# Performance work log

Hardware: AMD Instinct MI355X
Metric: run time of the kernel (lower is better)

Reference implementation:

```python
import jax, jax.numpy as jnp
import numpy as np

V, D, H, DH, FF, L = 512, 256, 8, 32, 2048, 2
B, S = 4, 128
EPS = 1e-5


def setup_inputs() -> dict:
    key = jax.random.key(0)
    ks = jax.random.split(key, 8)
    rn = lambda k, shape: jax.random.normal(k, shape, jnp.float32) * 0.02
    return {
        "x_t": jax.random.randint(ks[0], (B, S), 0, V),
        "emb": rn(ks[1], (V, D)),
        "temperature": jnp.array(1.0, jnp.float32),
        "Wq": rn(ks[2], (L, D, D)), "Wk": rn(ks[3], (L, D, D)),
        "Wv": rn(ks[4], (L, D, D)), "Wo": rn(ks[5], (L, D, D)),
        "bq": jnp.zeros((L, D)), "bk": jnp.zeros((L, D)),
        "bv": jnp.zeros((L, D)), "bo": jnp.zeros((L, D)),
        "W1": rn(ks[6], (L, D, FF)), "b1": jnp.zeros((L, FF)),
        "W2": rn(ks[7], (L, FF, D)), "b2": jnp.zeros((L, D)),
        "ln1_s": jnp.ones((L, D)), "ln1_b": jnp.zeros((L, D)),
        "ln2_s": jnp.ones((L, D)), "ln2_b": jnp.zeros((L, D)),
    }


def _layer_norm(x, scale, bias):
    m = jnp.mean(x, axis=-1, keepdims=True)
    v = jnp.var(x, axis=-1, keepdims=True)
    return (x - m) / jnp.sqrt(v + EPS) * scale + bias


def reference(x_t, emb, temperature, Wq, Wk, Wv, Wo, bq, bk, bv, bo,
              W1, b1, W2, b2, ln1_s, ln1_b, ln2_s, ln2_b):
    b, s = x_t.shape
    x = emb[x_t]  # [B,S,D]
    scale = 1.0 / np.sqrt(DH).astype(np.float32)
    for l in range(L):  # 2 structurally distinct layers (post-norm, ReLU FFN)
        q = (x @ Wq[l] + bq[l]).reshape(b, s, H, DH)
        k = (x @ Wk[l] + bk[l]).reshape(b, s, H, DH)
        v = (x @ Wv[l] + bv[l]).reshape(b, s, H, DH)
        scores = jnp.einsum('bqhd,bkhd->bhqk', q, k) * scale
        attn = jax.nn.softmax(scores, axis=-1)
        o = jnp.einsum('bhqk,bkhd->bqhd', attn, v).reshape(b, s, D)
        x = _layer_norm(x + (o @ Wo[l] + bo[l]), ln1_s[l], ln1_b[l])
        ff = jax.nn.relu(x @ W1[l] + b1[l]) @ W2[l] + b2[l]
        x = _layer_norm(x + ff, ln2_s[l], ln2_b[l])
    sim = (x @ emb.T) / temperature            # [B,S,V]
    tp = jax.nn.softmax(sim, axis=-1)          # [B,S,V]
    # torch loop `trans_matrix[:,:,i,:] = transition_probs` == broadcast over row dim
    return jnp.broadcast_to(tp[:, :, None, :], (b, s, V, V))
```

## Files before the change

### kernel.cpp

```cpp
#include <hip/hip_runtime.h>
#include <math.h>

#define V_  512
#define D_  256
#define H_  8
#define DH_ 32
#define FF_ 2048
#define L_  2
#define B_  4
#define S_  128
#define T_  (B_*S_)

typedef float f32x4 __attribute__((ext_vector_type(4)));
typedef short s16x8 __attribute__((ext_vector_type(8)));
typedef unsigned short u16x4 __attribute__((ext_vector_type(4)));
typedef unsigned short ushort_t;

__device__ __forceinline__ ushort_t f2b(float f) {
    unsigned int u = __builtin_bit_cast(unsigned int, f);
    u += 0x7FFFu + ((u >> 16) & 1u);
    return (ushort_t)(u >> 16);
}
__device__ __forceinline__ float b2f(ushort_t h) {
    unsigned int u = ((unsigned int)h) << 16;
    return __builtin_bit_cast(float, u);
}

__device__ __forceinline__ float waveReduceSum(float v) {
#pragma unroll
    for (int off = 32; off > 0; off >>= 1) v += __shfl_xor(v, off);
    return v;
}
__device__ __forceinline__ float waveReduceMax(float v) {
#pragma unroll
    for (int off = 32; off > 0; off >>= 1) v = fmaxf(v, __shfl_xor(v, off));
    return v;
}

template<int RELU, int OUTB, int BIAS>
__device__ __forceinline__ void mgemm_body(
    const ushort_t* __restrict__ A, const ushort_t* __restrict__ BT,
    const float* __restrict__ bias, float* __restrict__ Cf,
    ushort_t* __restrict__ Cb, int M, int N, int K, int kBegin, int kSteps)
{
    __shared__ ushort_t Al[2][64][72];
    __shared__ ushort_t Bl[2][64][72];
    const int tid  = threadIdx.x;
    const int m0   = blockIdx.y * 64, n0 = blockIdx.x * 64;
    const int lane = tid & 63, w = tid >> 6;
    const int srow = tid >> 2, sseg = (tid & 3) * 16;
    const int l15  = lane & 15,  kg = (lane >> 4) * 8;

    f32x4 acc0 = {0.f,0.f,0.f,0.f}, acc1 = acc0, acc2 = acc0, acc3 = acc0;

    const ushort_t* Aptr = &A [(size_t)(m0 + srow) * K + kBegin + sseg];
    const ushort_t* Bptr = &BT[(size_t)(n0 + srow) * K + kBegin + sseg];

    s16x8 av0 = *(const s16x8*)Aptr,       av1 = *(const s16x8*)(Aptr + 8);
    s16x8 bv0 = *(const s16x8*)Bptr,       bv1 = *(const s16x8*)(Bptr + 8);
    *(s16x8*)&Al[0][srow][sseg]     = av0;
    *(s16x8*)&Al[0][srow][sseg + 8] = av1;
    *(s16x8*)&Bl[0][srow][sseg]     = bv0;
    *(s16x8*)&Bl[0][srow][sseg + 8] = bv1;

    for (int kt = 0; kt < kSteps; ++kt) {
        const int cur = kt & 1;
        const bool more = (kt + 1 < kSteps);
        if (more) {
            const size_t o = (size_t)(kt + 1) * 64;
            av0 = *(const s16x8*)(Aptr + o);     av1 = *(const s16x8*)(Aptr + o + 8);
            bv0 = *(const s16x8*)(Bptr + o);     bv1 = *(const s16x8*)(Bptr + o + 8);
        }
        asm volatile("s_waitcnt lgkmcnt(0)\n\ts_barrier" ::: "memory");

        s16x8 b0 = *(const s16x8*)&Bl[cur][w * 16 + l15][kg];
        s16x8 b1 = *(const s16x8*)&Bl[cur][w * 16 + l15][kg + 32];
        s16x8 a00 = *(const s16x8*)&Al[cur][     l15][kg];
        s16x8 a01 = *(const s16x8*)&Al[cur][     l15][kg + 32];
        s16x8 a10 = *(const s16x8*)&Al[cur][16 + l15][kg];
        s16x8 a11 = *(const s16x8*)&Al[cur][16 + l15][kg + 32];
        s16x8 a20 = *(const s16x8*)&Al[cur][32 + l15][kg];
        s16x8 a21 = *(const s16x8*)&Al[cur][32 + l15][kg + 32];
        s16x8 a30 = *(const s16x8*)&Al[cur][48 + l15][kg];
        s16x8 a31 = *(const s16x8*)&Al[cur][48 + l15][kg + 32];
        acc0 = __builtin_amdgcn_mfma_f32_16x16x32_bf16(a00, b0, acc0, 0, 0, 0);
        acc1 = __builtin_amdgcn_mfma_f32_16x16x32_bf16(a10, b0, acc1, 0, 0, 0);
        acc2 = __builtin_amdgcn_mfma_f32_16x16x32_bf16(a20, b0, acc2, 0, 0, 0);
        acc3 = __builtin_amdgcn_mfma_f32_16x16x32_bf16(a30, b0, acc3, 0, 0, 0);
        acc0 = __builtin_amdgcn_mfma_f32_16x16x32_bf16(a01, b1, acc0, 0, 0, 0);
        acc1 = __builtin_amdgcn_mfma_f32_16x16x32_bf16(a11, b1, acc1, 0, 0, 0);
        acc2 = __builtin_amdgcn_mfma_f32_16x16x32_bf16(a21, b1, acc2, 0, 0, 0);
        acc3 = __builtin_amdgcn_mfma_f32_16x16x32_bf16(a31, b1, acc3, 0, 0, 0);

        if (more) {
            *(s16x8*)&Al[cur ^ 1][srow][sseg]     = av0;
            *(s16x8*)&Al[cur ^ 1][srow][sseg + 8] = av1;
            *(s16x8*)&Bl[cur ^ 1][srow][sseg]     = bv0;
            *(s16x8*)&Bl[cur ^ 1][srow][sseg + 8] = bv1;
        }
    }

    const int col = n0 + w * 16 + l15;
    const float bb = BIAS ? bias[col] : 0.f;
    f32x4 accs[4] = {acc0, acc1, acc2, acc3};
#pragma unroll
    for (int r = 0; r < 4; ++r) {
#pragma unroll
        for (int e = 0; e < 4; ++e) {
            const int row = m0 + r * 16 + (lane >> 4) * 4 + e;
            float v = accs[r][e] + bb;
            if (RELU) v = fmaxf(v, 0.f);
            if (OUTB) Cb[(size_t)row * N + col] = f2b(v);
            else      Cf[(size_t)row * N + col] = v;
        }
    }
}

template<int RELU, int OUTB, int BIAS>
__global__ __launch_bounds__(256) void mgemm_k(const ushort_t* A, const ushort_t* BT,
    const float* bias, float* Cf0, float* Cf1, ushort_t* Cb,
    int M, int N, int K, int kChunk)
{
    const int z = blockIdx.z;
    float* Cfz = nullptr;
    if (Cf0) Cfz = (z < 2) ? Cf0 + (size_t)z * M * N
                           : Cf1 + (size_t)(z - 2) * M * N;
    mgemm_body<RELU, OUTB, BIAS>(A, BT, bias, Cfz, Cb, M, N, K,
                                 z * kChunk, kChunk / 64);
}

__global__ __launch_bounds__(256) void qkv_k(const ushort_t* Xb, const ushort_t* WT,
    const float* bq, const float* bk, const float* bv,
    ushort_t* Qb, ushort_t* Kb, ushort_t* Vb)
{
    const int z = blockIdx.z;
    const ushort_t* bt = WT + (size_t)z * (D_ * D_);
    const float* bias; ushort_t* out;
    if (z == 0)      { bias = bq; out = Qb; }
    else if (z == 1) { bias = bk; out = Kb; }
    else             { bias = bv; out = Vb; }
    mgemm_body<0, 1, 1>(Xb, bt, bias, nullptr, out, T_, D_, D_, 0, D_ / 64);
}

__global__ __launch_bounds__(256) void prep_k(const int* __restrict__ xt,
    const float* __restrict__ emb, float* __restrict__ X,
    ushort_t* __restrict__ Xb, ushort_t* __restrict__ embB,
    const float* __restrict__ Wq, const float* __restrict__ Wk,
    const float* __restrict__ Wv, const float* __restrict__ Wo,
    const float* __restrict__ W1, const float* __restrict__ W2,
    ushort_t* __restrict__ WT, ushort_t* __restrict__ W1T, ushort_t* __restrict__ W2T)
{
    __shared__ float Tl[32][33];
    const int tid = threadIdx.x;
    if (blockIdx.x < 512) {
        const int idx = blockIdx.x * 256 + tid;
        const int t = idx >> 8, d = idx & 255;
        const float v = emb[(size_t)xt[t] * D_ + d];
        X[idx]  = v;
        Xb[idx] = f2b(v);
        embB[idx] = f2b(emb[idx]);
        return;
    }
    const int id = blockIdx.x - 512;
    const int l  = id >= 1280 ? 1 : 0;
    const int t  = id - l * 1280;
    const float* src; ushort_t* dst; int R, C, rt, ct;
    if (t < 256) {
        const int kind = t >> 6, tl = t & 63;
        const float* s0 = (kind == 0) ? Wq : (kind == 1) ? Wk : (kind == 2) ? Wv : Wo;
        src = s0 + (size_t)l * (D_ * D_);
        dst = WT + (size_t)l * (4 * D_ * D_) + (size_t)kind * (D_ * D_);
        R = D_; C = D_; rt = tl >> 3; ct = tl & 7;
    } else if (t < 768) {
        const int tl = t - 256;
        src = W1 + (size_t)l * (D_ * FF_); dst = W1T + (size_t)l * (D_ * FF_);
        R = D_; C = FF_; rt = tl >> 6; ct = tl & 63;
    } else {
        const int tl = t - 768;
        src = W2 + (size_t)l * (FF_ * D_); dst = W2T + (size_t)l * (FF_ * D_);
        R = FF_; C = D_; rt = tl >> 3; ct = tl & 7;
    }
    const int r = tid >> 3, c4 = (tid & 7) * 4;
    f32x4 v = *(const f32x4*)&src[(size_t)(rt * 32 + r) * C + ct * 32 + c4];
    Tl[r][c4] = v[0]; Tl[r][c4 + 1] = v[1]; Tl[r][c4 + 2] = v[2]; Tl[r][c4 + 3] = v[3];
    __syncthreads();
    u16x4 ov;
    ov[0] = f2b(Tl[c4 + 0][r]); ov[1] = f2b(Tl[c4 + 1][r]);
    ov[2] = f2b(Tl[c4 + 2][r]); ov[3] = f2b(Tl[c4 + 3][r]);
    *(u16x4*)&dst[(size_t)(ct * 32 + r) * R + rt * 32 + c4] = ov;
}

__global__ __launch_bounds__(256) void add_ln_k(
    const float* __restrict__ p0, const float* __restrict__ p1, int nparts,
    const float* __restrict__ bias, float* __restrict__ X,
    ushort_t* __restrict__ Xb, const float* __restrict__ s,
    const float* __restrict__ b)
{
    __shared__ float red[4];
    const int row = blockIdx.x, tid = threadIdx.x;
    const size_t off = (size_t)row * D_ + tid;
    const size_t TD = (size_t)T_ * D_;
    float a = X[off] + bias[tid] + p0[off];
    if (nparts >= 2) a += p0[TD + off];
    if (nparts == 4) a += p1[off] + p1[TD + off];

    float ws_ = waveReduceSum(a);
    if ((tid & 63) == 0) red[tid >> 6] = ws_;
    __syncthreads();
    const float mean = (red[0] + red[1] + red[2] + red[3]) * (1.f / D_);
    __syncthreads();
    const float d = a - mean;
    float vs = waveReduceSum(d * d);
    if ((tid & 63) == 0) red[tid >> 6] = vs;
    __syncthreads();
    const float var = (red[0] + red[1] + red[2] + red[3]) * (1.f / D_);
    const float y = d * rsqrtf(var + 1e-5f) * s[tid] + b[tid];
    X[off]  = y;
    Xb[off] = f2b(y);
}

__global__ __launch_bounds__(256) void attn_k(const ushort_t* __restrict__ Qb,
    const ushort_t* __restrict__ Kb, const ushort_t* __restrict__ Vb,
    ushort_t* __restrict__ Ob)
{
    __shared__ float Qs[32][36], Ks[128][36], Vs[128][36], Ps[32][132];
    const int bh = blockIdx.x, b = bh >> 3, h = bh & 7;
    const int i0 = blockIdx.y * 32;
    const int tid = threadIdx.x;

#pragma unroll
    for (int it = 0; it < 2; ++it) {
        const int g = it * 256 + tid;
        const int r = g >> 2, c8 = (g & 3) * 8;
        s16x8 kv = *(const s16x8*)&Kb[(size_t)(b * S_ + r) * D_ + h * DH_ + c8];
        s16x8 vv = *(const s16x8*)&Vb[(size_t)(b * S_ + r) * D_ + h * DH_ + c8];
        f32x4 klo = {b2f((ushort_t)kv[0]), b2f((ushort_t)kv[1]), b2f((ushort_t)kv[2]), b2f((ushort_t)kv[3])};
        f32x4 khi = {b2f((ushort_t)kv[4]), b2f((ushort_t)kv[5]), b2f((ushort_t)kv[6]), b2f((ushort_t)kv[7])};
        f32x4 vlo = {b2f((ushort_t)vv[0]), b2f((ushort_t)vv[1]), b2f((ushort_t)vv[2]), b2f((ushort_t)vv[3])};
        f32x4 vhi = {b2f((ushort_t)vv[4]), b2f((ushort_t)vv[5]), b2f((ushort_t)vv[6]), b2f((ushort_t)vv[7])};
        *(f32x4*)&Ks[r][c8]     = klo;  *(f32x4*)&Ks[r][c8 + 4] = khi;
        *(f32x4*)&Vs[r][c8]     = vlo;  *(f32x4*)&Vs[r][c8 + 4] = vhi;
    }
    if (tid < 128) {
        const int r = tid >> 2, c8 = (tid & 3) * 8;
        s16x8 qv = *(const s16x8*)&Qb[(size_t)(b * S_ + i0 + r) * D_ + h * DH_ + c8];
        f32x4 qlo = {b2f((ushort_t)qv[0]), b2f((ushort_t)qv[1]), b2f((ushort_t)qv[2]), b2f((ushort_t)qv[3])};
        f32x4 qhi = {b2f((ushort_t)qv[4]), b2f((ushort_t)qv[5]), b2f((ushort_t)qv[6]), b2f((ushort_t)qv[7])};
        *(f32x4*)&Qs[r][c8] = qlo;  *(f32x4*)&Qs[r][c8 + 4] = qhi;
    }
    __syncthreads();

    const int i = tid >> 3, jg = tid & 7;
    const float sc = 0.17677669529663687f;
    float sv[16];
    float mx = -1e30f;
#pragma unroll
    for (int jj = 0; jj < 16; ++jj) {
        const int j = jg + jj * 8;
        f32x4 a4 = {0.f,0.f,0.f,0.f};
#pragma unroll
        for (int kk = 0; kk < 8; ++kk) {
            f32x4 q = *(const f32x4*)&Qs[i][kk * 4];
            f32x4 k = *(const f32x4*)&Ks[j][kk * 4];
            a4 += q * k;
        }
        const float sdot = (a4[0] + a4[1] + a4[2] + a4[3]) * sc;
        sv[jj] = sdot;
        mx = fmaxf(mx, sdot);
    }
    mx = fmaxf(mx, __shfl_xor(mx, 1));
    mx = fmaxf(mx, __shfl_xor(mx, 2));
    mx = fmaxf(mx, __shfl_xor(mx, 4));
    float sum = 0.f;
#pragma unroll
    for (int jj = 0; jj < 16; ++jj) {
        const float e = __expf(sv[jj] - mx);
        Ps[i][jg + jj * 8] = e;
        sum += e;
    }
    sum += __shfl_xor(sum, 1);
    sum += __shfl_xor(sum, 2);
    sum += __shfl_xor(sum, 4);
    const float inv = 1.f / sum;
    __syncthreads();

    const int dg = tid & 7;
    f32x4 o = {0.f,0.f,0.f,0.f};
#pragma unroll 4
    for (int j = 0; j < 128; ++j) {
        const float p = Ps[i][j];
        f32x4 vv = *(const f32x4*)&Vs[j][dg * 4];
        o += vv * p;
    }
    u16x4 ov;
    ov[0] = f2b(o[0] * inv); ov[1] = f2b(o[1] * inv);
    ov[2] = f2b(o[2] * inv); ov[3] = f2b(o[3] * inv);
    *(u16x4*)&Ob[(size_t)(b * S_ + i0 + i) * D_ + h * DH_ + dg * 4] = ov;
}

__global__ __launch_bounds__(256) void bcast_k(const float* __restrict__ Lg,
    const float* __restrict__ temp, float* __restrict__ out)
{
    __shared__ float row[V_];
    __shared__ float red[4];
    const int blk = blockIdx.x, t = blk >> 2, quarter = blk & 3;
    const int tid = threadIdx.x;
    const float rT = 1.f / temp[0];
    const float l0 = Lg[(size_t)t * V_ + tid] * rT;
    const float l1 = Lg[(size_t)t * V_ + 256 + tid] * rT;
    float m = waveReduceMax(fmaxf(l0, l1));
    if ((tid & 63) == 0) red[tid >> 6] = m;
    __syncthreads();
    m = fmaxf(fmaxf(red[0], red[1]), fmaxf(red[2], red[3]));
    __syncthreads();
    const float e0 = __expf(l0 - m), e1 = __expf(l1 - m);
    float sblk = waveReduceSum(e0 + e1);
    if ((tid & 63) == 0) red[tid >> 6] = sblk;
    __syncthreads();
    const float inv = 1.f / (red[0] + red[1] + red[2] + red[3]);
    row[tid] = e0 * inv;
    row[tid + 256] = e1 * inv;
    __syncthreads();

    const int c = tid & 127, ihalf = tid >> 7;
    f32x4 v = *(const f32x4*)&row[c * 4];
    f32x4* dst = (f32x4*)out + (size_t)t * V_ * (V_ / 4);
#pragma unroll 4
    for (int r = 0; r < 64; ++r) {
        const int i = quarter * 128 + ihalf + r * 2;
        __builtin_nontemporal_store(v, &dst[(size_t)i * (V_ / 4) + c]);
    }
}

extern "C" void kernel_launch(void* const* d_in, const int* in_sizes, int n_in,
                              void* d_out, int out_size, void* d_ws, size_t ws_size,
                              hipStream_t stream)
{
    const int*   x_t  = (const int*)  d_in[0];
    const float* emb  = (const float*)d_in[1];
    const float* temp = (const float*)d_in[2];
    const float* Wq   = (const float*)d_in[3];
    const float* Wk   = (const float*)d_in[4];
    const float* Wv   = (const float*)d_in[5];
    const float* Wo   = (const float*)d_in[6];
    const float* bq   = (const float*)d_in[7];
    const float* bk   = (const float*)d_in[8];
    const float* bv   = (const float*)d_in[9];
    const float* bo   = (const float*)d_in[10];
    const float* W1   = (const float*)d_in[11];
    const float* b1   = (const float*)d_in[12];
    const float* W2   = (const float*)d_in[13];
    const float* b2   = (const float*)d_in[14];
    const float* ln1s = (const float*)d_in[15];
    const float* ln1b = (const float*)d_in[16];
    const float* ln2s = (const float*)d_in[17];
    const float* ln2b = (const float*)d_in[18];

    float* out = (float*)d_out;
    char*  wsb = (char*)d_ws;

    float*    X     = (float*)   (wsb + 0);
    float*    PartA = (float*)   (wsb + 524288);
    float*    Lg    = PartA;
    ushort_t* Qb    = (ushort_t*)(wsb + 1572864);
    float*    PartB = (float*)   (wsb + 1572864);
    ushort_t* Kb    = (ushort_t*)(wsb + 1835008);
    ushort_t* Vb    = (ushort_t*)(wsb + 2097152);
    ushort_t* Ob    = (ushort_t*)(wsb + 2359296);
    ushort_t* Xb    = (ushort_t*)(wsb + 2621440);
    ushort_t* Ffb   = (ushort_t*)(wsb + 2883584);
    ushort_t* embB  = (ushort_t*)(wsb + 4980736);
    ushort_t* WT    = (ushort_t*)(wsb + 5242880);
    ushort_t* W1T   = (ushort_t*)(wsb + 6291456);
    ushort_t* W2T   = (ushort_t*)(wsb + 8388608);

    prep_k<<<3072, 256, 0, stream>>>(x_t, emb, X, Xb, embB,
                                     Wq, Wk, Wv, Wo, W1, W2, WT, W1T, W2T);

    for (int l = 0; l < L_; ++l) {
        const ushort_t* WTl  = WT  + (size_t)l * (4 * D_ * D_);
        const ushort_t* W1Tl = W1T + (size_t)l * (D_ * FF_);
        const ushort_t* W2Tl = W2T + (size_t)l * (FF_ * D_);

        qkv_k<<<dim3(4, 8, 3), 256, 0, stream>>>(
            Xb, WTl, bq + l * D_, bk + l * D_, bv + l * D_, Qb, Kb, Vb);

        attn_k<<<dim3(32, 4), 256, 0, stream>>>(Qb, Kb, Vb, Ob);

        mgemm_k<0, 0, 0><<<dim3(4, 8, 2), 256, 0, stream>>>(
            Ob, WTl + 3 * D_ * D_, nullptr, PartA, nullptr, nullptr,
            T_, D_, D_, D_ / 2);
        add_ln_k<<<T_, 256, 0, stream>>>(PartA, nullptr, 2, bo + l * D_,
                                         X, Xb, ln1s + l * D_, ln1b + l * D_);

        mgemm_k<1, 1, 1><<<dim3(32, 8, 1), 256, 0, stream>>>(
            Xb, W1Tl, b1 + l * FF_, nullptr, nullptr, Ffb, T_, FF_, D_, D_);

        mgemm_k<0, 0, 0><<<dim3(4, 8, 4), 256, 0, stream>>>(
            Ffb, W2Tl, nullptr, PartA, PartB, nullptr, T_, D_, FF_, FF_ / 4);
        add_ln_k<<<T_, 256, 0, stream>>>(PartA, PartB, 4, b2 + l * D_,
                                         X, Xb, ln2s + l * D_, ln2b + l * D_);
    }

    mgemm_k<0, 0, 0><<<dim3(8, 8, 1), 256, 0, stream>>>(
        Xb, embB, nullptr, Lg, nullptr, nullptr, T_, V_, D_, D_);

    bcast_k<<<T_ * 4, 256, 0, stream>>>(Lg, temp, out);
}
```

Baseline: 172.6 us.

## Fuse QKV projection into attention and Wo GEMM into residual LayerNorm

```diff
diff --git a/kernel.cpp b/kernel.cpp
--- a/kernel.cpp
+++ b/kernel.cpp
@@ -129,17 +129,183 @@
                                  z * kChunk, kChunk / 64);
 }
 
-__global__ __launch_bounds__(256) void qkv_k(const ushort_t* Xb, const ushort_t* WT,
-    const float* bq, const float* bk, const float* bv,
-    ushort_t* Qb, ushort_t* Kb, ushort_t* Vb)
-{
-    const int z = blockIdx.z;
-    const ushort_t* bt = WT + (size_t)z * (D_ * D_);
-    const float* bias; ushort_t* out;
-    if (z == 0)      { bias = bq; out = Qb; }
-    else if (z == 1) { bias = bk; out = Kb; }
-    else             { bias = bv; out = Vb; }
-    mgemm_body<0, 1, 1>(Xb, bt, bias, nullptr, out, T_, D_, D_, 0, D_ / 64);
+__global__ __launch_bounds__(512) void qkvattn_k(
+    const ushort_t* __restrict__ Xb, const ushort_t* __restrict__ WT,
+    const float* __restrict__ bq, const float* __restrict__ bk,
+    const float* __restrict__ bv, ushort_t* __restrict__ Ob)
+{
+    __shared__ float Qs[128][36], Ks[128][36], Vs[128][36];
+    const int bh = blockIdx.x, b = bh >> 3, h = bh & 7;
+    const int tid = threadIdx.x;
+    const int w = tid >> 6, lane = tid & 63;
+    const int l15 = lane & 15, kg = (lane >> 4) * 8;
+
+    {
+        const ushort_t* WB; const float* bias; float (*dst)[36];
+        int rowbase, nrf;
+        if (w < 4)      { WB = WT;               bias = bq; dst = Qs; rowbase = w * 32;       nrf = 2; }
+        else if (w < 6) { WB = WT + D_ * D_;     bias = bk; dst = Ks; rowbase = (w - 4) * 64; nrf = 4; }
+        else            { WB = WT + 2 * D_ * D_; bias = bv; dst = Vs; rowbase = (w - 6) * 64; nrf = 4; }
+
+        f32x4 acc[4][2] = {};
+        const ushort_t* Abase = Xb + (size_t)(b * S_ + rowbase) * D_;
+        const ushort_t* Bbase = WB + (size_t)(h * DH_) * D_;
+#pragma unroll
+        for (int kk = 0; kk < 8; ++kk) {
+            const int k0 = kk * 32 + kg;
+            s16x8 bf0 = *(const s16x8*)&Bbase[(size_t)l15 * D_ + k0];
+            s16x8 bf1 = *(const s16x8*)&Bbase[(size_t)(16 + l15) * D_ + k0];
+#pragma unroll
+            for (int rf = 0; rf < 4; ++rf) {
+                if (rf < nrf) {
+                    s16x8 af = *(const s16x8*)&Abase[(size_t)(rf * 16 + l15) * D_ + k0];
+                    acc[rf][0] = __builtin_amdgcn_mfma_f32_16x16x32_bf16(af, bf0, acc[rf][0], 0, 0, 0);
+                    acc[rf][1] = __builtin_amdgcn_mfma_f32_16x16x32_bf16(af, bf1, acc[rf][1], 0, 0, 0);
+                }
+            }
+        }
+        const int r0 = (lane >> 4) * 4;
+#pragma unroll
+        for (int rf = 0; rf < 4; ++rf) {
+            if (rf < nrf) {
+#pragma unroll
+                for (int cf = 0; cf < 2; ++cf) {
+                    const int col = cf * 16 + l15;
+                    const float bb = bias[h * DH_ + col];
+#pragma unroll
+                    for (int e = 0; e < 4; ++e)
+                        dst[rowbase + rf * 16 + r0 + e][col] = acc[rf][cf][e] + bb;
+                }
+            }
+        }
+    }
+    __syncthreads();
+
+    const int i = tid >> 2, jg = tid & 3;
+    const float sc = 0.17677669529663687f;
+    float p[32];
+    float mx = -1e30f;
+#pragma unroll
+    for (int jj = 0; jj < 32; ++jj) {
+        const int j = jg + jj * 4;
+        f32x4 a4 = {0.f, 0.f, 0.f, 0.f};
+#pragma unroll
+        for (int k4 = 0; k4 < 8; ++k4) {
+            f32x4 q  = *(const f32x4*)&Qs[i][k4 * 4];
+            f32x4 kv = *(const f32x4*)&Ks[j][k4 * 4];
+            a4 += q * kv;
+        }
+        const float s = (a4[0] + a4[1] + a4[2] + a4[3]) * sc;
+        p[jj] = s;
+        mx = fmaxf(mx, s);
+    }
+    mx = fmaxf(mx, __shfl_xor(mx, 1));
+    mx = fmaxf(mx, __shfl_xor(mx, 2));
+    float sum = 0.f;
+#pragma unroll
+    for (int jj = 0; jj < 32; ++jj) {
+        p[jj] = __expf(p[jj] - mx);
+        sum += p[jj];
+    }
+    sum += __shfl_xor(sum, 1);
+    sum += __shfl_xor(sum, 2);
+    const float inv = 1.f / sum;
+
+    f32x4 o[8] = {};
+#pragma unroll
+    for (int jj = 0; jj < 32; ++jj) {
+        const int j = jg + jj * 4;
+        const float pv = p[jj];
+#pragma unroll
+        for (int d4 = 0; d4 < 8; ++d4) {
+            f32x4 vv = *(const f32x4*)&Vs[j][d4 * 4];
+            o[d4] += vv * pv;
+        }
+    }
+#pragma unroll
+    for (int d4 = 0; d4 < 8; ++d4) {
+#pragma unroll
+        for (int e = 0; e < 4; ++e) {
+            o[d4][e] += __shfl_xor(o[d4][e], 1);
+            o[d4][e] += __shfl_xor(o[d4][e], 2);
+        }
+    }
+    const int d0 = jg * 2;
+    s16x8 ov;
+#pragma unroll
+    for (int e = 0; e < 4; ++e) {
+        ov[e]     = (short)f2b(o[d0][e] * inv);
+        ov[4 + e] = (short)f2b(o[d0 + 1][e] * inv);
+    }
+    *(s16x8*)&Ob[(size_t)(b * S_ + i) * D_ + h * DH_ + jg * 8] = ov;
+}
+
+__global__ __launch_bounds__(512) void woln_k(
+    const ushort_t* __restrict__ A,
+    const ushort_t* __restrict__ BT,
+    const float* __restrict__ bias,
+    float* __restrict__ X, ushort_t* __restrict__ Xb,
+    const float* __restrict__ lns, const float* __restrict__ lnb)
+{
+    __shared__ float Ct[16][264];
+    const int tid = threadIdx.x;
+    const int m0 = blockIdx.x * 16;
+    const int w = tid >> 6, lane = tid & 63;
+    const int l15 = lane & 15, kg = (lane >> 4) * 8;
+
+    f32x4 acc0 = {0.f,0.f,0.f,0.f}, acc1 = acc0;
+    const ushort_t* Abase = A  + (size_t)(m0 + l15) * D_;
+    const ushort_t* B0    = BT + (size_t)(w * 32 + l15) * D_;
+    const ushort_t* B1    = BT + (size_t)(w * 32 + 16 + l15) * D_;
+#pragma unroll
+    for (int kk = 0; kk < 8; ++kk) {
+        const int k0 = kk * 32 + kg;
+        s16x8 af = *(const s16x8*)&Abase[k0];
+        s16x8 b0 = *(const s16x8*)&B0[k0];
+        s16x8 b1 = *(const s16x8*)&B1[k0];
+        acc0 = __builtin_amdgcn_mfma_f32_16x16x32_bf16(af, b0, acc0, 0, 0, 0);
+        acc1 = __builtin_amdgcn_mfma_f32_16x16x32_bf16(af, b1, acc1, 0, 0, 0);
+    }
+    const int r0 = (lane >> 4) * 4;
+#pragma unroll
+    for (int e = 0; e < 4; ++e) {
+        Ct[r0 + e][w * 32 + l15]      = acc0[e];
+        Ct[r0 + e][w * 32 + 16 + l15] = acc1[e];
+    }
+    __syncthreads();
+
+    const int row = tid >> 5, cg = tid & 31;
+    const int grow = m0 + row, c0 = cg * 8;
+    float a[8];
+    float sum = 0.f;
+#pragma unroll
+    for (int e = 0; e < 8; ++e) {
+        a[e] = Ct[row][c0 + e] + X[(size_t)grow * D_ + c0 + e] + bias[c0 + e];
+        sum += a[e];
+    }
+    sum += __shfl_xor(sum, 1);  sum += __shfl_xor(sum, 2);
+    sum += __shfl_xor(sum, 4);  sum += __shfl_xor(sum, 8);
+    sum += __shfl_xor(sum, 16);
+    const float mean = sum * (1.f / D_);
+    float vs = 0.f;
+#pragma unroll
+    for (int e = 0; e < 8; ++e) { const float d = a[e] - mean; vs += d * d; }
+    vs += __shfl_xor(vs, 1);  vs += __shfl_xor(vs, 2);
+    vs += __shfl_xor(vs, 4);  vs += __shfl_xor(vs, 8);
+    vs += __shfl_xor(vs, 16);
+    const float rstd = rsqrtf(vs * (1.f / D_) + 1e-5f);
+    f32x4 y0, y1; u16x4 yb0, yb1;
+#pragma unroll
+    for (int e = 0; e < 4; ++e) {
+        const float ya = (a[e] - mean) * rstd * lns[c0 + e] + lnb[c0 + e];
+        const float yc = (a[e + 4] - mean) * rstd * lns[c0 + 4 + e] + lnb[c0 + 4 + e];
+        y0[e] = ya; yb0[e] = f2b(ya);
+        y1[e] = yc; yb1[e] = f2b(yc);
+    }
+    *(f32x4*)&X [(size_t)grow * D_ + c0]     = y0;
+    *(f32x4*)&X [(size_t)grow * D_ + c0 + 4] = y1;
+    *(u16x4*)&Xb[(size_t)grow * D_ + c0]     = yb0;
+    *(u16x4*)&Xb[(size_t)grow * D_ + c0 + 4] = yb1;
 }
 
 __global__ __launch_bounds__(256) void prep_k(const int* __restrict__ xt,
@@ -217,85 +383,6 @@
     const float y = d * rsqrtf(var + 1e-5f) * s[tid] + b[tid];
     X[off]  = y;
     Xb[off] = f2b(y);
-}
-
-__global__ __launch_bounds__(256) void attn_k(const ushort_t* __restrict__ Qb,
-    const ushort_t* __restrict__ Kb, const ushort_t* __restrict__ Vb,
-    ushort_t* __restrict__ Ob)
-{
-    __shared__ float Qs[32][36], Ks[128][36], Vs[128][36], Ps[32][132];
-    const int bh = blockIdx.x, b = bh >> 3, h = bh & 7;
-    const int i0 = blockIdx.y * 32;
-    const int tid = threadIdx.x;
-
-#pragma unroll
-    for (int it = 0; it < 2; ++it) {
-        const int g = it * 256 + tid;
-        const int r = g >> 2, c8 = (g & 3) * 8;
-        s16x8 kv = *(const s16x8*)&Kb[(size_t)(b * S_ + r) * D_ + h * DH_ + c8];
-        s16x8 vv = *(const s16x8*)&Vb[(size_t)(b * S_ + r) * D_ + h * DH_ + c8];
-        f32x4 klo = {b2f((ushort_t)kv[0]), b2f((ushort_t)kv[1]), b2f((ushort_t)kv[2]), b2f((ushort_t)kv[3])};
-        f32x4 khi = {b2f((ushort_t)kv[4]), b2f((ushort_t)kv[5]), b2f((ushort_t)kv[6]), b2f((ushort_t)kv[7])};
-        f32x4 vlo = {b2f((ushort_t)vv[0]), b2f((ushort_t)vv[1]), b2f((ushort_t)vv[2]), b2f((ushort_t)vv[3])};
-        f32x4 vhi = {b2f((ushort_t)vv[4]), b2f((ushort_t)vv[5]), b2f((ushort_t)vv[6]), b2f((ushort_t)vv[7])};
-        *(f32x4*)&Ks[r][c8]     = klo;  *(f32x4*)&Ks[r][c8 + 4] = khi;
-        *(f32x4*)&Vs[r][c8]     = vlo;  *(f32x4*)&Vs[r][c8 + 4] = vhi;
-    }
-    if (tid < 128) {
-        const int r = tid >> 2, c8 = (tid & 3) * 8;
-        s16x8 qv = *(const s16x8*)&Qb[(size_t)(b * S_ + i0 + r) * D_ + h * DH_ + c8];
-        f32x4 qlo = {b2f((ushort_t)qv[0]), b2f((ushort_t)qv[1]), b2f((ushort_t)qv[2]), b2f((ushort_t)qv[3])};
-        f32x4 qhi = {b2f((ushort_t)qv[4]), b2f((ushort_t)qv[5]), b2f((ushort_t)qv[6]), b2f((ushort_t)qv[7])};
-        *(f32x4*)&Qs[r][c8] = qlo;  *(f32x4*)&Qs[r][c8 + 4] = qhi;
-    }
-    __syncthreads();
-
-    const int i = tid >> 3, jg = tid & 7;
-    const float sc = 0.17677669529663687f;
-    float sv[16];
-    float mx = -1e30f;
-#pragma unroll
-    for (int jj = 0; jj < 16; ++jj) {
-        const int j = jg + jj * 8;
-        f32x4 a4 = {0.f,0.f,0.f,0.f};
-#pragma unroll
-        for (int kk = 0; kk < 8; ++kk) {
-            f32x4 q = *(const f32x4*)&Qs[i][kk * 4];
-            f32x4 k = *(const f32x4*)&Ks[j][kk * 4];
-            a4 += q * k;
-        }
-        const float sdot = (a4[0] + a4[1] + a4[2] + a4[3]) * sc;
-        sv[jj] = sdot;
-        mx = fmaxf(mx, sdot);
-    }
-    mx = fmaxf(mx, __shfl_xor(mx, 1));
-    mx = fmaxf(mx, __shfl_xor(mx, 2));
-    mx = fmaxf(mx, __shfl_xor(mx, 4));
-    float sum = 0.f;
-#pragma unroll
-    for (int jj = 0; jj < 16; ++jj) {
-        const float e = __expf(sv[jj] - mx);
-        Ps[i][jg + jj * 8] = e;
-        sum += e;
-    }
-    sum += __shfl_xor(sum, 1);
-    sum += __shfl_xor(sum, 2);
-    sum += __shfl_xor(sum, 4);
-    const float inv = 1.f / sum;
-    __syncthreads();
-
-    const int dg = tid & 7;
-    f32x4 o = {0.f,0.f,0.f,0.f};
-#pragma unroll 4
-    for (int j = 0; j < 128; ++j) {
-        const float p = Ps[i][j];
-        f32x4 vv = *(const f32x4*)&Vs[j][dg * 4];
-        o += vv * p;
-    }
-    u16x4 ov;
-    ov[0] = f2b(o[0] * inv); ov[1] = f2b(o[1] * inv);
-    ov[2] = f2b(o[2] * inv); ov[3] = f2b(o[3] * inv);
-    *(u16x4*)&Ob[(size_t)(b * S_ + i0 + i) * D_ + h * DH_ + dg * 4] = ov;
 }
 
 __global__ __launch_bounds__(256) void bcast_k(const float* __restrict__ Lg,
@@ -362,10 +449,7 @@
     float*    X     = (float*)   (wsb + 0);
     float*    PartA = (float*)   (wsb + 524288);
     float*    Lg    = PartA;
-    ushort_t* Qb    = (ushort_t*)(wsb + 1572864);
     float*    PartB = (float*)   (wsb + 1572864);
-    ushort_t* Kb    = (ushort_t*)(wsb + 1835008);
-    ushort_t* Vb    = (ushort_t*)(wsb + 2097152);
     ushort_t* Ob    = (ushort_t*)(wsb + 2359296);
     ushort_t* Xb    = (ushort_t*)(wsb + 2621440);
     ushort_t* Ffb   = (ushort_t*)(wsb + 2883584);
@@ -382,16 +466,11 @@
         const ushort_t* W1Tl = W1T + (size_t)l * (D_ * FF_);
         const ushort_t* W2Tl = W2T + (size_t)l * (FF_ * D_);
 
-        qkv_k<<<dim3(4, 8, 3), 256, 0, stream>>>(
-            Xb, WTl, bq + l * D_, bk + l * D_, bv + l * D_, Qb, Kb, Vb);
-
-        attn_k<<<dim3(32, 4), 256, 0, stream>>>(Qb, Kb, Vb, Ob);
-
-        mgemm_k<0, 0, 0><<<dim3(4, 8, 2), 256, 0, stream>>>(
-            Ob, WTl + 3 * D_ * D_, nullptr, PartA, nullptr, nullptr,
-            T_, D_, D_, D_ / 2);
-        add_ln_k<<<T_, 256, 0, stream>>>(PartA, nullptr, 2, bo + l * D_,
-                                         X, Xb, ln1s + l * D_, ln1b + l * D_);
+        qkvattn_k<<<32, 512, 0, stream>>>(
+            Xb, WTl, bq + l * D_, bk + l * D_, bv + l * D_, Ob);
+
+        woln_k<<<32, 512, 0, stream>>>(Ob, WTl + 3 * D_ * D_, bo + l * D_,
+                                       X, Xb, ln1s + l * D_, ln1b + l * D_);
 
         mgemm_k<1, 1, 1><<<dim3(32, 8, 1), 256, 0, stream>>>(
             Xb, W1Tl, b1 + l * FF_, nullptr, nullptr, Ffb, T_, FF_, D_, D_);
```

Measured after the change: 201.3 us. 16.6% more time.

## Fuse residual-add LayerNorm into following GEMM prologues, drop add_ln kernels

Applied to the files above, without the earlier changes.

```diff
diff --git a/kernel.cpp b/kernel.cpp
--- a/kernel.cpp
+++ b/kernel.cpp
@@ -38,15 +38,18 @@
 }
 
 template<int RELU, int OUTB, int BIAS>
-__device__ __forceinline__ void mgemm_body(
-    const ushort_t* __restrict__ A, const ushort_t* __restrict__ BT,
-    const float* __restrict__ bias, float* __restrict__ Cf,
-    ushort_t* __restrict__ Cb, int M, int N, int K, int kBegin, int kSteps)
+__global__ __launch_bounds__(256) void mgemm_k(const ushort_t* __restrict__ A,
+    const ushort_t* __restrict__ BT, const float* __restrict__ bias,
+    float* __restrict__ Cf0, ushort_t* __restrict__ Cb,
+    int M, int N, int K, int kChunk)
 {
     __shared__ ushort_t Al[2][64][72];
     __shared__ ushort_t Bl[2][64][72];
     const int tid  = threadIdx.x;
     const int m0   = blockIdx.y * 64, n0 = blockIdx.x * 64;
+    const int z    = blockIdx.z;
+    const int kBegin = z * kChunk, kSteps = kChunk / 64;
+    float* Cf = Cf0 ? Cf0 + (size_t)z * M * N : nullptr;
     const int lane = tid & 63, w = tid >> 6;
     const int srow = tid >> 2, sseg = (tid & 3) * 16;
     const int l15  = lane & 15,  kg = (lane >> 4) * 8;
@@ -56,8 +59,8 @@
     const ushort_t* Aptr = &A [(size_t)(m0 + srow) * K + kBegin + sseg];
     const ushort_t* Bptr = &BT[(size_t)(n0 + srow) * K + kBegin + sseg];
 
-    s16x8 av0 = *(const s16x8*)Aptr,       av1 = *(const s16x8*)(Aptr + 8);
-    s16x8 bv0 = *(const s16x8*)Bptr,       bv1 = *(const s16x8*)(Bptr + 8);
+    s16x8 av0 = *(const s16x8*)Aptr,  av1 = *(const s16x8*)(Aptr + 8);
+    s16x8 bv0 = *(const s16x8*)Bptr,  bv1 = *(const s16x8*)(Bptr + 8);
     *(s16x8*)&Al[0][srow][sseg]     = av0;
     *(s16x8*)&Al[0][srow][sseg + 8] = av1;
     *(s16x8*)&Bl[0][srow][sseg]     = bv0;
@@ -73,8 +76,8 @@
         }
         asm volatile("s_waitcnt lgkmcnt(0)\n\ts_barrier" ::: "memory");
 
-        s16x8 b0 = *(const s16x8*)&Bl[cur][w * 16 + l15][kg];
-        s16x8 b1 = *(const s16x8*)&Bl[cur][w * 16 + l15][kg + 32];
+        s16x8 b0  = *(const s16x8*)&Bl[cur][w * 16 + l15][kg];
+        s16x8 b1  = *(const s16x8*)&Bl[cur][w * 16 + l15][kg + 32];
         s16x8 a00 = *(const s16x8*)&Al[cur][     l15][kg];
         s16x8 a01 = *(const s16x8*)&Al[cur][     l15][kg + 32];
         s16x8 a10 = *(const s16x8*)&Al[cur][16 + l15][kg];
@@ -116,35 +119,174 @@
     }
 }
 
-template<int RELU, int OUTB, int BIAS>
-__global__ __launch_bounds__(256) void mgemm_k(const ushort_t* A, const ushort_t* BT,
-    const float* bias, float* Cf0, float* Cf1, ushort_t* Cb,
-    int M, int N, int K, int kChunk)
-{
-    const int z = blockIdx.z;
-    float* Cfz = nullptr;
-    if (Cf0) Cfz = (z < 2) ? Cf0 + (size_t)z * M * N
-                           : Cf1 + (size_t)(z - 2) * M * N;
-    mgemm_body<RELU, OUTB, BIAS>(A, BT, bias, Cfz, Cb, M, N, K,
-                                 z * kChunk, kChunk / 64);
-}
-
-__global__ __launch_bounds__(256) void qkv_k(const ushort_t* Xb, const ushort_t* WT,
-    const float* bq, const float* bk, const float* bv,
-    ushort_t* Qb, ushort_t* Kb, ushort_t* Vb)
+template<int NPARTS, int RELU, int OUTB, int BIAS>
+__device__ __forceinline__ void gemmln_body(
+    const float* __restrict__ Xres, const float* __restrict__ p0,
+    const float* __restrict__ addb, const float* __restrict__ lns,
+    const float* __restrict__ lnb,
+    const ushort_t* __restrict__ BT, const float* __restrict__ gbias,
+    float* __restrict__ Cf, ushort_t* __restrict__ Cb,
+    float* __restrict__ Xout, int m0, int n0, int N)
+{
+    __shared__ ushort_t At[64][264];
+    __shared__ ushort_t Bl[2][64][72];
+    const int tid = threadIdx.x;
+    const int lane = tid & 63, w = tid >> 6;
+    const int l15 = lane & 15, kg = (lane >> 4) * 8;
+    const size_t TD = (size_t)T_ * D_;
+
+    {
+        const int r = tid >> 2, q = tid & 3;
+        const int grow = m0 + r;
+        const float* xrow = Xres + (size_t)grow * D_;
+        f32x4 a[16];
+        float s = 0.f, s2 = 0.f;
+#pragma unroll
+        for (int i = 0; i < 16; ++i) {
+            const int c = (i << 4) + (q << 2);
+            f32x4 v = *(const f32x4*)&xrow[c];
+            if (NPARTS >= 2) {
+                v += *(const f32x4*)&addb[c];
+                v += *(const f32x4*)&p0[(size_t)grow * D_ + c];
+                v += *(const f32x4*)&p0[TD + (size_t)grow * D_ + c];
+            }
+            a[i] = v;
+            s  += v[0] + v[1] + v[2] + v[3];
+            s2 += v[0]*v[0] + v[1]*v[1] + v[2]*v[2] + v[3]*v[3];
+        }
+        float mean = 0.f, rstd = 1.f;
+        if (NPARTS) {
+            s  += __shfl_xor(s, 1);  s  += __shfl_xor(s, 2);
+            s2 += __shfl_xor(s2, 1); s2 += __shfl_xor(s2, 2);
+            mean = s * (1.f / D_);
+            const float var = s2 * (1.f / D_) - mean * mean;
+            rstd = rsqrtf(var + 1e-5f);
+        }
+        const bool wr = (Xout != nullptr);
+#pragma unroll
+        for (int i = 0; i < 16; ++i) {
+            const int c = (i << 4) + (q << 2);
+            f32x4 y;
+            if (NPARTS) {
+#pragma unroll
+                for (int e = 0; e < 4; ++e)
+                    y[e] = (a[i][e] - mean) * rstd * lns[c + e] + lnb[c + e];
+            } else y = a[i];
+            u16x4 yb;
+#pragma unroll
+            for (int e = 0; e < 4; ++e) yb[e] = f2b(y[e]);
+            *(u16x4*)&At[r][c] = yb;
+            if (wr) *(f32x4*)&Xout[(size_t)grow * D_ + c] = y;
+        }
+    }
+
+    const int srow = tid >> 2, sseg = (tid & 3) * 16;
+    const ushort_t* Bptr = &BT[(size_t)(n0 + srow) * D_ + sseg];
+    s16x8 bv0 = *(const s16x8*)Bptr, bv1 = *(const s16x8*)(Bptr + 8);
+    *(s16x8*)&Bl[0][srow][sseg]     = bv0;
+    *(s16x8*)&Bl[0][srow][sseg + 8] = bv1;
+
+    f32x4 acc0 = {0.f,0.f,0.f,0.f}, acc1 = acc0, acc2 = acc0, acc3 = acc0;
+#pragma unroll
+    for (int kt = 0; kt < 4; ++kt) {
+        const int cur = kt & 1;
+        if (kt < 3) {
+            const size_t o = (size_t)(kt + 1) * 64;
+            bv0 = *(const s16x8*)(Bptr + o);  bv1 = *(const s16x8*)(Bptr + o + 8);
+        }
+        asm volatile("s_waitcnt lgkmcnt(0)\n\ts_barrier" ::: "memory");
+
+        const int k0 = kt * 64;
+        s16x8 b0  = *(const s16x8*)&Bl[cur][w * 16 + l15][kg];
+        s16x8 b1  = *(const s16x8*)&Bl[cur][w * 16 + l15][kg + 32];
+        s16x8 a00 = *(const s16x8*)&At[     l15][k0 + kg];
+        s16x8 a01 = *(const s16x8*)&At[     l15][k0 + kg + 32];
+        s16x8 a10 = *(const s16x8*)&At[16 + l15][k0 + kg];
+        s16x8 a11 = *(const s16x8*)&At[16 + l15][k0 + kg + 32];
+        s16x8 a20 = *(const s16x8*)&At[32 + l15][k0 + kg];
+        s16x8 a21 = *(const s16x8*)&At[32 + l15][k0 + kg + 32];
+        s16x8 a30 = *(const s16x8*)&At[48 + l15][k0 + kg];
+        s16x8 a31 = *(const s16x8*)&At[48 + l15][k0 + kg + 32];
+        acc0 = __builtin_amdgcn_mfma_f32_16x16x32_bf16(a00, b0, acc0, 0, 0, 0);
+        acc1 = __builtin_amdgcn_mfma_f32_16x16x32_bf16(a10, b0, acc1, 0, 0, 0);
+        acc2 = __builtin_amdgcn_mfma_f32_16x16x32_bf16(a20, b0, acc2, 0, 0, 0);
+        acc3 = __builtin_amdgcn_mfma_f32_16x16x32_bf16(a30, b0, acc3, 0, 0, 0);
+        acc0 = __builtin_amdgcn_mfma_f32_16x16x32_bf16(a01, b1, acc0, 0, 0, 0);
+        acc1 = __builtin_amdgcn_mfma_f32_16x16x32_bf16(a11, b1, acc1, 0, 0, 0);
+        acc2 = __builtin_amdgcn_mfma_f32_16x16x32_bf16(a21, b1, acc2, 0, 0, 0);
+        acc3 = __builtin_amdgcn_mfma_f32_16x16x32_bf16(a31, b1, acc3, 0, 0, 0);
+
+        if (kt < 3) {
+            *(s16x8*)&Bl[cur ^ 1][srow][sseg]     = bv0;
+            *(s16x8*)&Bl[cur ^ 1][srow][sseg + 8] = bv1;
+        }
+    }
+
+    const int col = n0 + w * 16 + l15;
+    const float bb = BIAS ? gbias[col] : 0.f;
+    f32x4 accs[4] = {acc0, acc1, acc2, acc3};
+#pragma unroll
+    for (int r = 0; r < 4; ++r) {
+#pragma unroll
+        for (int e = 0; e < 4; ++e) {
+            const int row = m0 + r * 16 + (lane >> 4) * 4 + e;
+            float v = accs[r][e] + bb;
+            if (RELU) v = fmaxf(v, 0.f);
+            if (OUTB) Cb[(size_t)row * N + col] = f2b(v);
+            else      Cf[(size_t)row * N + col] = v;
+        }
+    }
+}
+
+template<int NPARTS>
+__global__ __launch_bounds__(256) void qkvln_k(
+    const float* __restrict__ Xres, const float* __restrict__ p0,
+    const float* __restrict__ addb, const float* __restrict__ lns,
+    const float* __restrict__ lnb, const ushort_t* __restrict__ WT,
+    const float* __restrict__ bq, const float* __restrict__ bk,
+    const float* __restrict__ bv,
+    ushort_t* __restrict__ Qb, ushort_t* __restrict__ Kb,
+    ushort_t* __restrict__ Vb, float* __restrict__ Xout)
 {
     const int z = blockIdx.z;
     const ushort_t* bt = WT + (size_t)z * (D_ * D_);
-    const float* bias; ushort_t* out;
-    if (z == 0)      { bias = bq; out = Qb; }
-    else if (z == 1) { bias = bk; out = Kb; }
-    else             { bias = bv; out = Vb; }
-    mgemm_body<0, 1, 1>(Xb, bt, bias, nullptr, out, T_, D_, D_, 0, D_ / 64);
+    const float* bias; ushort_t* outp;
+    if (z == 0)      { bias = bq; outp = Qb; }
+    else if (z == 1) { bias = bk; outp = Kb; }
+    else             { bias = bv; outp = Vb; }
+    float* xo = (z == 0 && blockIdx.x == 0) ? Xout : nullptr;
+    gemmln_body<NPARTS, 0, 1, 1>(Xres, p0, addb, lns, lnb, bt, bias,
+                                 nullptr, outp, xo,
+                                 blockIdx.y * 64, blockIdx.x * 64, D_);
+}
+
+__global__ __launch_bounds__(256) void w1ln_k(
+    const float* __restrict__ Xres, const float* __restrict__ p0,
+    const float* __restrict__ addb, const float* __restrict__ lns,
+    const float* __restrict__ lnb, const ushort_t* __restrict__ W1T,
+    const float* __restrict__ b1, ushort_t* __restrict__ Ffb,
+    float* __restrict__ Xout)
+{
+    float* xo = (blockIdx.x == 0) ? Xout : nullptr;
+    gemmln_body<2, 1, 1, 1>(Xres, p0, addb, lns, lnb, W1T, b1,
+                            nullptr, Ffb, xo,
+                            blockIdx.y * 64, blockIdx.x * 64, FF_);
+}
+
+__global__ __launch_bounds__(256) void logitsln_k(
+    const float* __restrict__ Xres, const float* __restrict__ p0,
+    const float* __restrict__ addb, const float* __restrict__ lns,
+    const float* __restrict__ lnb, const ushort_t* __restrict__ embB,
+    float* __restrict__ Lg)
+{
+    gemmln_body<2, 0, 0, 0>(Xres, p0, addb, lns, lnb, embB, nullptr,
+                            Lg, nullptr, nullptr,
+                            blockIdx.y * 64, blockIdx.x * 64, V_);
 }
 
 __global__ __launch_bounds__(256) void prep_k(const int* __restrict__ xt,
     const float* __restrict__ emb, float* __restrict__ X,
-    ushort_t* __restrict__ Xb, ushort_t* __restrict__ embB,
+    ushort_t* __restrict__ embB,
     const float* __restrict__ Wq, const float* __restrict__ Wk,
     const float* __restrict__ Wv, const float* __restrict__ Wo,
     const float* __restrict__ W1, const float* __restrict__ W2,
@@ -155,9 +297,7 @@
     if (blockIdx.x < 512) {
         const int idx = blockIdx.x * 256 + tid;
         const int t = idx >> 8, d = idx & 255;
-        const float v = emb[(size_t)xt[t] * D_ + d];
-        X[idx]  = v;
-        Xb[idx] = f2b(v);
+        X[idx]  = emb[(size_t)xt[t] * D_ + d];
         embB[idx] = f2b(emb[idx]);
         return;
     }
@@ -188,35 +328,6 @@
     ov[0] = f2b(Tl[c4 + 0][r]); ov[1] = f2b(Tl[c4 + 1][r]);
     ov[2] = f2b(Tl[c4 + 2][r]); ov[3] = f2b(Tl[c4 + 3][r]);
     *(u16x4*)&dst[(size_t)(ct * 32 + r) * R + rt * 32 + c4] = ov;
-}
-
-__global__ __launch_bounds__(256) void add_ln_k(
-    const float* __restrict__ p0, const float* __restrict__ p1, int nparts,
-    const float* __restrict__ bias, float* __restrict__ X,
-    ushort_t* __restrict__ Xb, const float* __restrict__ s,
-    const float* __restrict__ b)
-{
-    __shared__ float red[4];
-    const int row = blockIdx.x, tid = threadIdx.x;
-    const size_t off = (size_t)row * D_ + tid;
-    const size_t TD = (size_t)T_ * D_;
-    float a = X[off] + bias[tid] + p0[off];
-    if (nparts >= 2) a += p0[TD + off];
-    if (nparts == 4) a += p1[off] + p1[TD + off];
-
-    float ws_ = waveReduceSum(a);
-    if ((tid & 63) == 0) red[tid >> 6] = ws_;
-    __syncthreads();
-    const float mean = (red[0] + red[1] + red[2] + red[3]) * (1.f / D_);
-    __syncthreads();
-    const float d = a - mean;
-    float vs = waveReduceSum(d * d);
-    if ((tid & 63) == 0) red[tid >> 6] = vs;
-    __syncthreads();
-    const float var = (red[0] + red[1] + red[2] + red[3]) * (1.f / D_);
-    const float y = d * rsqrtf(var + 1e-5f) * s[tid] + b[tid];
-    X[off]  = y;
-    Xb[off] = f2b(y);
 }
 
 __global__ __launch_bounds__(256) void attn_k(const ushort_t* __restrict__ Qb,
@@ -359,51 +470,67 @@
     float* out = (float*)d_out;
     char*  wsb = (char*)d_ws;
 
-    float*    X     = (float*)   (wsb + 0);
-    float*    PartA = (float*)   (wsb + 524288);
-    float*    Lg    = PartA;
-    ushort_t* Qb    = (ushort_t*)(wsb + 1572864);
-    float*    PartB = (float*)   (wsb + 1572864);
-    ushort_t* Kb    = (ushort_t*)(wsb + 1835008);
-    ushort_t* Vb    = (ushort_t*)(wsb + 2097152);
-    ushort_t* Ob    = (ushort_t*)(wsb + 2359296);
-    ushort_t* Xb    = (ushort_t*)(wsb + 2621440);
-    ushort_t* Ffb   = (ushort_t*)(wsb + 2883584);
-    ushort_t* embB  = (ushort_t*)(wsb + 4980736);
-    ushort_t* WT    = (ushort_t*)(wsb + 5242880);
-    ushort_t* W1T   = (ushort_t*)(wsb + 6291456);
-    ushort_t* W2T   = (ushort_t*)(wsb + 8388608);
-
-    prep_k<<<3072, 256, 0, stream>>>(x_t, emb, X, Xb, embB,
+    float*    XA    = (float*)   (wsb + 0);
+    float*    XB    = (float*)   (wsb + 524288);
+    float*    PartA = (float*)   (wsb + 1048576);
+    ushort_t* Qb    = (ushort_t*)(wsb + 2097152);
+    ushort_t* Kb    = (ushort_t*)(wsb + 2359296);
+    ushort_t* Vb    = (ushort_t*)(wsb + 2621440);
+    ushort_t* Ob    = (ushort_t*)(wsb + 2883584);
+    float*    Lg    = (float*)   (wsb + 2097152);
+    ushort_t* Ffb   = (ushort_t*)(wsb + 3145728);
+    ushort_t* embB  = (ushort_t*)(wsb + 5242880);
+    ushort_t* WT    = (ushort_t*)(wsb + 5505024);
+    ushort_t* W1T   = (ushort_t*)(wsb + 6553600);
+    ushort_t* W2T   = (ushort_t*)(wsb + 8650752);
+
+    prep_k<<<3072, 256, 0, stream>>>(x_t, emb, XA, embB,
                                      Wq, Wk, Wv, Wo, W1, W2, WT, W1T, W2T);
 
-    for (int l = 0; l < L_; ++l) {
-        const ushort_t* WTl  = WT  + (size_t)l * (4 * D_ * D_);
-        const ushort_t* W1Tl = W1T + (size_t)l * (D_ * FF_);
-        const ushort_t* W2Tl = W2T + (size_t)l * (FF_ * D_);
-
-        qkv_k<<<dim3(4, 8, 3), 256, 0, stream>>>(
-            Xb, WTl, bq + l * D_, bk + l * D_, bv + l * D_, Qb, Kb, Vb);
+    {
+        const ushort_t* WT0  = WT;
+        const ushort_t* W1T0 = W1T;
+        const ushort_t* W2T0 = W2T;
+
+        qkvln_k<0><<<dim3(4, 8, 3), 256, 0, stream>>>(
+            XA, nullptr, nullptr, nullptr, nullptr, WT0,
+            bq, bk, bv, Qb, Kb, Vb, nullptr);
 
         attn_k<<<dim3(32, 4), 256, 0, stream>>>(Qb, Kb, Vb, Ob);
 
         mgemm_k<0, 0, 0><<<dim3(4, 8, 2), 256, 0, stream>>>(
-            Ob, WTl + 3 * D_ * D_, nullptr, PartA, nullptr, nullptr,
-            T_, D_, D_, D_ / 2);
-        add_ln_k<<<T_, 256, 0, stream>>>(PartA, nullptr, 2, bo + l * D_,
-                                         X, Xb, ln1s + l * D_, ln1b + l * D_);
-
-        mgemm_k<1, 1, 1><<<dim3(32, 8, 1), 256, 0, stream>>>(
-            Xb, W1Tl, b1 + l * FF_, nullptr, nullptr, Ffb, T_, FF_, D_, D_);
-
-        mgemm_k<0, 0, 0><<<dim3(4, 8, 4), 256, 0, stream>>>(
-            Ffb, W2Tl, nullptr, PartA, PartB, nullptr, T_, D_, FF_, FF_ / 4);
-        add_ln_k<<<T_, 256, 0, stream>>>(PartA, PartB, 4, b2 + l * D_,
-                                         X, Xb, ln2s + l * D_, ln2b + l * D_);
-    }
-
-    mgemm_k<0, 0, 0><<<dim3(8, 8, 1), 256, 0, stream>>>(
-        Xb, embB, nullptr, Lg, nullptr, nullptr, T_, V_, D_, D_);
+            Ob, WT0 + 3 * D_ * D_, nullptr, PartA, nullptr, T_, D_, D_, D_ / 2);
+
+        w1ln_k<<<dim3(32, 8), 256, 0, stream>>>(
+            XA, PartA, bo, ln1s, ln1b, W1T0, b1, Ffb, XB);
+
+        mgemm_k<0, 0, 0><<<dim3(4, 8, 2), 256, 0, stream>>>(
+            Ffb, W2T0, nullptr, PartA, nullptr, T_, D_, FF_, FF_ / 2);
+    }
+
+    {
+        const ushort_t* WT1  = WT  + 4 * D_ * D_;
+        const ushort_t* W1T1 = W1T + D_ * FF_;
+        const ushort_t* W2T1 = W2T + FF_ * D_;
+
+        qkvln_k<2><<<dim3(4, 8, 3), 256, 0, stream>>>(
+            XB, PartA, b2, ln2s, ln2b, WT1,
+            bq + D_, bk + D_, bv + D_, Qb, Kb, Vb, XA);
+
+        attn_k<<<dim3(32, 4), 256, 0, stream>>>(Qb, Kb, Vb, Ob);
+
+        mgemm_k<0, 0, 0><<<dim3(4, 8, 2), 256, 0, stream>>>(
+            Ob, WT1 + 3 * D_ * D_, nullptr, PartA, nullptr, T_, D_, D_, D_ / 2);
+
+        w1ln_k<<<dim3(32, 8), 256, 0, stream>>>(
+            XA, PartA, bo + D_, ln1s + D_, ln1b + D_, W1T1, b1 + FF_, Ffb, XB);
+
+        mgemm_k<0, 0, 0><<<dim3(4, 8, 2), 256, 0, stream>>>(
+            Ffb, W2T1, nullptr, PartA, nullptr, T_, D_, FF_, FF_ / 2);
+    }
+
+    logitsln_k<<<dim3(8, 8), 256, 0, stream>>>(
+        XB, PartA, b2 + D_, ln2s + D_, ln2b + D_, embB, Lg);
 
     bcast_k<<<T_ * 4, 256, 0, stream>>>(Lg, temp, out);
 }
```

Result: slower. 195.8 us (+13.4%).
